# Kernel optimization log

Measured on AMD Instinct MI355X. Metric: run time of the kernel, lower is better.

The kernel has to match this reference:

```python
import jax, jax.numpy as jnp
import numpy as np

B, S, O = 65536, 32, 16  # batch, state_dim, observation_dim


def setup_inputs() -> dict:
    key = jax.random.key(0)
    k1, k2, k3, k4 = jax.random.split(key, 4)
    observation = jax.random.normal(k1, (B, O), dtype=jnp.float32)
    # SPD observation noise covariance per batch element
    L = 0.1 * jax.random.normal(k2, (B, O, O), dtype=jnp.float32)
    observation_noise = jnp.einsum('bij,bkj->bik', L, L) + 1e-3 * jnp.eye(O, dtype=jnp.float32)
    observation_matrix = 0.001 * jax.random.normal(k3, (O, S), dtype=jnp.float32)
    observation_bias = 1e-6 * jax.random.normal(k4, (O,), dtype=jnp.float32)
    prior_mean = jnp.zeros((S,), dtype=jnp.float32)
    prior_precision = jnp.eye(S, dtype=jnp.float32)
    return {
        'observation': observation,
        'observation_noise': observation_noise,
        'observation_matrix': observation_matrix,
        'observation_bias': observation_bias,
        'prior_mean': prior_mean,
        'prior_precision': prior_precision,
    }


def reference(observation, observation_noise, observation_matrix, observation_bias,
              prior_mean, prior_precision):
    # observation: [B, O]; observation_noise: [B, O, O]
    noise_prec = jnp.linalg.inv(observation_noise)                      # [B, O, O]
    HtR = jnp.einsum('os,bop->bsp', observation_matrix, noise_prec)     # H^T R^{-1}: [B, S, O]
    innovation_cov = jnp.einsum('bso,ot->bst', HtR, observation_matrix) # [B, S, S]
    posterior_covariance = jnp.linalg.inv(prior_precision + innovation_cov)  # [B, S, S]
    residual = jnp.einsum('bso,bo->bs', HtR, observation - observation_bias)[..., None]  # [B, S, 1]
    prior_term = (prior_precision @ prior_mean)[:, None]                # [S, 1]
    posterior_mean = posterior_covariance @ (prior_term + residual)     # [B, S, 1]
    return posterior_mean, posterior_covariance
```

## Files before the change

kernel.cpp:

```cpp
#include <hip/hip_runtime.h>
#include <hip/hip_bf16.h>


typedef __attribute__((ext_vector_type(8))) short bf16x8;
typedef __attribute__((ext_vector_type(4))) float f32x4;

__device__ __forceinline__ unsigned bf16rne(float f) {
    unsigned x = __float_as_uint(f);
    return (x + 0x7FFFu + ((x >> 16) & 1u)) >> 16;
}
__device__ __forceinline__ unsigned pack2(float a, float b) {
    return bf16rne(a) | (bf16rne(b) << 16);
}

__global__ void lgs_setup(const float* __restrict__ H, const float* __restrict__ bias,
                          const float* __restrict__ mu0, const float* __restrict__ P,
                          float* __restrict__ ws)
{
    __shared__ float aug[32][65];
    __shared__ float colk[32];
    __shared__ float Gs[16][32];
    __shared__ float Gts[32][16];
    const int tid = threadIdx.x;

    for (int idx = tid; idx < 2048; idx += 256) {
        int r = idx >> 6, c = idx & 63;
        aug[r][c] = (c < 32) ? P[r * 32 + c] : (((c - 32) == r) ? 1.0f : 0.0f);
    }
    __syncthreads();

    for (int k = 0; k < 32; ++k) {
        if (tid < 32) colk[tid] = aug[tid][k];
        __syncthreads();
        if (tid < 64) {
            float rk = aug[k][tid] * (1.0f / colk[k]);
            aug[k][tid] = rk;
            for (int r = 0; r < 32; ++r)
                if (r != k) aug[r][tid] -= colk[r] * rk;
        }
        __syncthreads();
    }

    for (int idx = tid; idx < 512; idx += 256) {
        int o = idx >> 5, s = idx & 31;
        float acc = 0.f;
        for (int v = 0; v < 32; ++v) acc += H[o * 32 + v] * aug[v][32 + s];
        Gs[o][s] = acc;
    }
    for (int idx = tid; idx < 512; idx += 256) {
        int s = idx >> 4, o = idx & 15;
        float acc = 0.f;
        for (int v = 0; v < 32; ++v) acc += aug[s][32 + v] * H[o * 32 + v];
        Gts[s][o] = acc;
    }
    __syncthreads();

    for (int idx = tid; idx < 256; idx += 256) {
        int j = idx >> 4, i = idx & 15;
        float acc = 0.f;
        for (int s = 0; s < 32; ++s) acc += Gs[i][s] * H[j * 32 + s];
        ws[idx] = acc;
    }
    unsigned* wsu = (unsigned*)ws;
    for (int idx = tid; idx < 512; idx += 256) {
        int r = idx >> 8, rem = idx & 255;
        int l = rem >> 2, j = rem & 3;
        int mm = 16 * r + (l & 15);
        int kb = (((l >> 4) * 8) + 2 * j) & 15;
        wsu[768 + idx] = pack2(0.5f * Gts[mm][kb], 0.5f * Gts[mm][kb + 1]);
    }
    for (int idx = tid; idx < 1024; idx += 256) {
        int tt = idx >> 8, rem = idx & 255;
        int l = rem >> 2, j = rem & 3;
        int row = 16 * (tt >> 1) + ((l >> 4) << 2) + j;
        int col = 16 * (tt & 1) + (l & 15);
        ws[1280 + idx] = aug[row][32 + col];
    }
    for (int idx = tid; idx < 512; idx += 256) {
        int c = idx >> 8, rem = idx & 255;
        int l = rem >> 2, j2 = rem & 3;
        int col = 16 * c + (l & 15);
        int k = (((l >> 4) * 8) + 2 * j2) & 15;
        wsu[2304 + idx] = pack2(0.5f * Gs[k][col], 0.5f * Gs[k + 1][col]);
    }
    if (tid < 16) {
        float acc = bias[tid];
        for (int s = 0; s < 32; ++s) acc += H[tid * 32 + s] * mu0[s];
        ws[2816 + tid] = acc;
    }
    if (tid < 32) ws[2832 + tid] = mu0[tid];
}

#define BCAST8(x, K) __int_as_float(__builtin_amdgcn_ds_swizzle(__float_as_int(x), (((K) << 5) | 0x18)))

template <int K>
__device__ __forceinline__ void sweep_step(int l, float (&m0)[16], float (&m1)[16])
{
    const bool own = (l & 7) == (K & 7);
    float (&mp)[16] = (K >> 3) ? m1 : m0;
    float (&mo)[16] = (K >> 3) ? m0 : m1;
    if (own) mp[K] = 1.0f / mp[K];
    float bc[16];
#pragma unroll
    for (int i = 0; i < 16; ++i) bc[i] = BCAST8(mp[i], K & 7);
    float fp = own ? 0.0f : mp[K] * bc[K];
    float fo = mo[K] * bc[K];
#pragma unroll
    for (int i = 0; i < 16; ++i) {
        if (i != K) { mp[i] -= bc[i] * fp; mo[i] -= bc[i] * fo; }
    }
    mp[K] = fp;
    mo[K] = fo;
    if (own) {
        float invd = bc[K];
#pragma unroll
        for (int i = 0; i < 16; ++i) mp[i] = bc[i] * invd;
        mp[K] = -invd;
    }
}

__global__ __launch_bounds__(512, 2) void lgs_main(
    const float* __restrict__ obs, const float* __restrict__ noise,
    const float* __restrict__ ws,
    float* __restrict__ out_mean, float* __restrict__ out_cov, int B)
{
    __shared__ unsigned ldu[8192];

    const int tid  = threadIdx.x;
    const int l    = tid & 63;
    const int wv   = tid >> 6;
    const int g    = l & 7;
    const int slot = wv * 8 + (l >> 3);
    const int b    = blockIdx.x * 64 + slot;
    const int bb   = (b < B) ? b : (B - 1);

    const float* __restrict__ Acm  = ws;
    const float* __restrict__ cvec = ws + 2816;
    const float* __restrict__ m0v  = ws + 2832;

    float m0[16], m1[16];

    const float4* Rr0 = (const float4*)(noise + (size_t)bb * 256 + g * 16);
    const float4* Ar0 = (const float4*)(Acm + g * 16);
    const float4* Rr1 = (const float4*)(noise + (size_t)bb * 256 + (g + 8) * 16);
    const float4* Ar1 = (const float4*)(Acm + (g + 8) * 16);
#pragma unroll
    for (int i = 0; i < 4; ++i) {
        float4 r = Rr0[i], a = Ar0[i];
        m0[4*i+0] = r.x + a.x; m0[4*i+1] = r.y + a.y;
        m0[4*i+2] = r.z + a.z; m0[4*i+3] = r.w + a.w;
        float4 r1 = Rr1[i], a1 = Ar1[i];
        m1[4*i+0] = r1.x + a1.x; m1[4*i+1] = r1.y + a1.y;
        m1[4*i+2] = r1.z + a1.z; m1[4*i+3] = r1.w + a1.w;
    }

    sweep_step<0>(l, m0, m1);   sweep_step<1>(l, m0, m1);
    sweep_step<2>(l, m0, m1);   sweep_step<3>(l, m0, m1);
    sweep_step<4>(l, m0, m1);   sweep_step<5>(l, m0, m1);
    sweep_step<6>(l, m0, m1);   sweep_step<7>(l, m0, m1);
    sweep_step<8>(l, m0, m1);   sweep_step<9>(l, m0, m1);
    sweep_step<10>(l, m0, m1);  sweep_step<11>(l, m0, m1);
    sweep_step<12>(l, m0, m1);  sweep_step<13>(l, m0, m1);
    sweep_step<14>(l, m0, m1);  sweep_step<15>(l, m0, m1);

    {
        unsigned* qb = &ldu[slot * 128 + g * 8];
        const int x0 = g & 4;
        *(uint4*)&qb[x0]      = make_uint4(pack2(m0[0],m0[1]),  pack2(m0[2],m0[3]),
                                           pack2(m0[4],m0[5]),  pack2(m0[6],m0[7]));
        *(uint4*)&qb[x0 ^ 4]  = make_uint4(pack2(m0[8],m0[9]),  pack2(m0[10],m0[11]),
                                           pack2(m0[12],m0[13]), pack2(m0[14],m0[15]));
        *(uint4*)&qb[64 + x0] = make_uint4(pack2(m1[0],m1[1]),  pack2(m1[2],m1[3]),
                                           pack2(m1[4],m1[5]),  pack2(m1[6],m1[7]));
        *(uint4*)&qb[64 + (x0 ^ 4)] = make_uint4(pack2(m1[8],m1[9]),  pack2(m1[10],m1[11]),
                                                 pack2(m1[12],m1[13]), pack2(m1[14],m1[15]));
    }
    asm volatile("" ::: "memory");

    const uint4*  AF4 = (const uint4*)(ws + 768);
    const uint4*  BG4 = (const uint4*)(ws + 2304);
    const float4* PF4 = (const float4*)(ws + 1280);
    uint4 a0u = AF4[l], a1u = AF4[64 + l];
    uint4 g0u = BG4[l], g1u = BG4[64 + l];
    bf16x8 A0, A1, Bg0, Bg1;
    __builtin_memcpy(&A0,  &a0u, 16);
    __builtin_memcpy(&A1,  &a1u, 16);
    __builtin_memcpy(&Bg0, &g0u, 16);
    __builtin_memcpy(&Bg1, &g1u, 16);

    const int ch   = l & 15;
    const int gp   = l >> 4;
    const int qoff = ch * 8 + (((gp & 1) * 4) ^ (ch & 4));
    const int xt   = (ch & 1) << 2;
    const int g2   = gp * 2;
    const int kp   = (gp & 1) * 4;
    const float4 cv = ((const float4*)cvec)[gp];
    const float mu0a = m0v[ch], mu0b = m0v[16 + ch];
    const f32x4 zero = {0.f, 0.f, 0.f, 0.f};

#pragma unroll
    for (int h = 0; h < 8; ++h) {
        const int sh  = wv * 8 + h;
        const int bh  = blockIdx.x * 64 + sh;
        const int bhc = (bh < B) ? bh : (B - 1);
        unsigned* tb = &ldu[sh * 128];

        uint4 qu = *(const uint4*)&tb[qoff];
        bf16x8 Qa; __builtin_memcpy(&Qa, &qu, 16);
        f32x4 d0 = __builtin_amdgcn_mfma_f32_16x16x32_bf16(Qa, Bg0, zero, 0, 0, 0);
        f32x4 d1 = __builtin_amdgcn_mfma_f32_16x16x32_bf16(Qa, Bg1, zero, 0, 0, 0);

        float4 yv = *(const float4*)(obs + (size_t)bhc * 16 + gp * 4);
        float z0 = cv.x - yv.x, z1 = cv.y - yv.y, z2 = cv.z - yv.z, z3 = cv.w - yv.w;
        float p0 = d0[0]*z0 + d0[1]*z1 + d0[2]*z2 + d0[3]*z3;
        float p1 = d1[0]*z0 + d1[1]*z1 + d1[2]*z2 + d1[3]*z3;
        p0 += __int_as_float(__builtin_amdgcn_ds_swizzle(__float_as_int(p0), 0x401F));
        p1 += __int_as_float(__builtin_amdgcn_ds_swizzle(__float_as_int(p1), 0x401F));
        p0 += __shfl_xor(p0, 32, 64);
        p1 += __shfl_xor(p1, 32, 64);
        if (bh < B) {
            if (gp == 0) out_mean[(size_t)bh * 32 + ch]      = mu0a + p0;
            if (gp == 1) out_mean[(size_t)bh * 32 + 16 + ch] = mu0b + p1;
        }

        asm volatile("" ::: "memory");
        *(uint2*)&tb[ch * 8 + (g2 ^ xt)] =
            make_uint2(pack2(d0[0], d0[1]), pack2(d0[2], d0[3]));
        asm volatile("" ::: "memory");
        uint4 bu0 = *(const uint4*)&tb[ch * 8 + (kp ^ xt)];
        bf16x8 Bf0; __builtin_memcpy(&Bf0, &bu0, 16);
        float4 pq0 = PF4[l];
        float4 pq2 = PF4[128 + l];
        f32x4 pfr0; pfr0[0]=pq0.x; pfr0[1]=pq0.y; pfr0[2]=pq0.z; pfr0[3]=pq0.w;
        f32x4 pfr2; pfr2[0]=pq2.x; pfr2[1]=pq2.y; pfr2[2]=pq2.z; pfr2[3]=pq2.w;
        f32x4 s00 = __builtin_amdgcn_mfma_f32_16x16x32_bf16(A0, Bf0, pfr0, 0, 0, 0);
        f32x4 s10 = __builtin_amdgcn_mfma_f32_16x16x32_bf16(A1, Bf0, pfr2, 0, 0, 0);

        asm volatile("" ::: "memory");
        *(uint2*)&tb[ch * 8 + (g2 ^ xt)] =
            make_uint2(pack2(d1[0], d1[1]), pack2(d1[2], d1[3]));
        asm volatile("" ::: "memory");
        uint4 bu1 = *(const uint4*)&tb[ch * 8 + (kp ^ xt)];
        bf16x8 Bf1; __builtin_memcpy(&Bf1, &bu1, 16);
        float4 pq1 = PF4[64 + l];
        float4 pq3 = PF4[192 + l];
        f32x4 pfr1; pfr1[0]=pq1.x; pfr1[1]=pq1.y; pfr1[2]=pq1.z; pfr1[3]=pq1.w;
        f32x4 pfr3; pfr3[0]=pq3.x; pfr3[1]=pq3.y; pfr3[2]=pq3.z; pfr3[3]=pq3.w;
        f32x4 s01 = __builtin_amdgcn_mfma_f32_16x16x32_bf16(A0, Bf1, pfr1, 0, 0, 0);
        f32x4 s11 = __builtin_amdgcn_mfma_f32_16x16x32_bf16(A1, Bf1, pfr3, 0, 0, 0);
        asm volatile("" ::: "memory");

        if (bh < B) {
            float* Sb = out_cov + (size_t)bh * 1024 + (gp * 4) * 32 + ch;
#pragma unroll
            for (int j = 0; j < 4; ++j) {
                Sb[j * 32]       = s00[j];
                Sb[j * 32 + 16]  = s01[j];
                Sb[j * 32 + 512] = s10[j];
                Sb[j * 32 + 528] = s11[j];
            }
        }
    }
}

extern "C" void kernel_launch(void* const* d_in, const int* in_sizes, int n_in,
                              void* d_out, int out_size, void* d_ws, size_t ws_size,
                              hipStream_t stream)
{
    const float* obs   = (const float*)d_in[0];
    const float* noise = (const float*)d_in[1];
    const float* H     = (const float*)d_in[2];
    const float* bias  = (const float*)d_in[3];
    const float* mu0   = (const float*)d_in[4];
    const float* P     = (const float*)d_in[5];
    float* ws = (float*)d_ws;

    const int B = in_sizes[0] / 16;
    float* out_mean = (float*)d_out;
    float* out_cov  = out_mean + (size_t)B * 32;

    lgs_setup<<<1, 256, 0, stream>>>(H, bias, mu0, P, ws);
    lgs_main<<<(B + 63) / 64, 512, 0, stream>>>(obs, noise, ws, out_mean, out_cov, B);
}
```

Measured before the change: 119.9 us.

## Write covariance transposed as float4 stores and double-buffer LDS staging

Because the posterior covariance is symmetric, each lane now writes the transposed MFMA output tile as contiguous float4 rows instead of scattered scalar stores at a 32-float stride. A separate per-wave LDS region holds both bf16 B-operand tiles, so the two pack/store/load rounds and their compiler barriers collapse into one, and all four MFMAs issue together. The mean output becomes a single masked store per wave. The exchange is extra LDS per block, which could affect occupancy, and a reliance on the computed matrix being close enough to symmetric that writing its transpose is acceptable.

Measured after the change: 124.4 us. 3.8% more time.

```diff
diff --git a/kernel.cpp b/kernel.cpp
--- a/kernel.cpp
+++ b/kernel.cpp
@@ -124,7 +124,7 @@
     const float* __restrict__ ws,
     float* __restrict__ out_mean, float* __restrict__ out_cov, int B)
 {
-    __shared__ unsigned ldu[8192];
+    __shared__ unsigned ldu[10240];
 
     const int tid  = threadIdx.x;
     const int l    = tid & 63;
@@ -197,6 +197,7 @@
     const float4 cv = ((const float4*)cvec)[gp];
     const float mu0a = m0v[ch], mu0b = m0v[16 + ch];
     const f32x4 zero = {0.f, 0.f, 0.f, 0.f};
+    unsigned* tw = &ldu[8192 + wv * 256];
 
 #pragma unroll
     for (int h = 0; h < 8; ++h) {
@@ -218,47 +219,46 @@
         p1 += __int_as_float(__builtin_amdgcn_ds_swizzle(__float_as_int(p1), 0x401F));
         p0 += __shfl_xor(p0, 32, 64);
         p1 += __shfl_xor(p1, 32, 64);
-        if (bh < B) {
-            if (gp == 0) out_mean[(size_t)bh * 32 + ch]      = mu0a + p0;
-            if (gp == 1) out_mean[(size_t)bh * 32 + 16 + ch] = mu0b + p1;
+        if (bh < B && l < 32) {
+            float muv = (l < 16) ? (mu0a + p0) : (mu0b + p1);
+            out_mean[(size_t)bh * 32 + l] = muv;
         }
 
-        asm volatile("" ::: "memory");
-        *(uint2*)&tb[ch * 8 + (g2 ^ xt)] =
+        *(uint2*)&tw[ch * 8 + (g2 ^ xt)] =
             make_uint2(pack2(d0[0], d0[1]), pack2(d0[2], d0[3]));
-        asm volatile("" ::: "memory");
-        uint4 bu0 = *(const uint4*)&tb[ch * 8 + (kp ^ xt)];
-        bf16x8 Bf0; __builtin_memcpy(&Bf0, &bu0, 16);
-        float4 pq0 = PF4[l];
-        float4 pq2 = PF4[128 + l];
-        f32x4 pfr0; pfr0[0]=pq0.x; pfr0[1]=pq0.y; pfr0[2]=pq0.z; pfr0[3]=pq0.w;
-        f32x4 pfr2; pfr2[0]=pq2.x; pfr2[1]=pq2.y; pfr2[2]=pq2.z; pfr2[3]=pq2.w;
-        f32x4 s00 = __builtin_amdgcn_mfma_f32_16x16x32_bf16(A0, Bf0, pfr0, 0, 0, 0);
-        f32x4 s10 = __builtin_amdgcn_mfma_f32_16x16x32_bf16(A1, Bf0, pfr2, 0, 0, 0);
-
-        asm volatile("" ::: "memory");
-        *(uint2*)&tb[ch * 8 + (g2 ^ xt)] =
+        *(uint2*)&tw[128 + ch * 8 + (g2 ^ xt)] =
             make_uint2(pack2(d1[0], d1[1]), pack2(d1[2], d1[3]));
         asm volatile("" ::: "memory");
-        uint4 bu1 = *(const uint4*)&tb[ch * 8 + (kp ^ xt)];
-        bf16x8 Bf1; __builtin_memcpy(&Bf1, &bu1, 16);
+        uint4 bu0 = *(const uint4*)&tw[ch * 8 + (kp ^ xt)];
+        uint4 bu1 = *(const uint4*)&tw[128 + ch * 8 + (kp ^ xt)];
+        bf16x8 Bf0, Bf1;
+        __builtin_memcpy(&Bf0, &bu0, 16);
+        __builtin_memcpy(&Bf1, &bu1, 16);
+
+        float4 pq0 = PF4[l];
         float4 pq1 = PF4[64 + l];
+        float4 pq2 = PF4[128 + l];
         float4 pq3 = PF4[192 + l];
+        f32x4 pfr0; pfr0[0]=pq0.x; pfr0[1]=pq0.y; pfr0[2]=pq0.z; pfr0[3]=pq0.w;
         f32x4 pfr1; pfr1[0]=pq1.x; pfr1[1]=pq1.y; pfr1[2]=pq1.z; pfr1[3]=pq1.w;
+        f32x4 pfr2; pfr2[0]=pq2.x; pfr2[1]=pq2.y; pfr2[2]=pq2.z; pfr2[3]=pq2.w;
         f32x4 pfr3; pfr3[0]=pq3.x; pfr3[1]=pq3.y; pfr3[2]=pq3.z; pfr3[3]=pq3.w;
+        f32x4 s00 = __builtin_amdgcn_mfma_f32_16x16x32_bf16(A0, Bf0, pfr0, 0, 0, 0);
         f32x4 s01 = __builtin_amdgcn_mfma_f32_16x16x32_bf16(A0, Bf1, pfr1, 0, 0, 0);
+        f32x4 s10 = __builtin_amdgcn_mfma_f32_16x16x32_bf16(A1, Bf0, pfr2, 0, 0, 0);
         f32x4 s11 = __builtin_amdgcn_mfma_f32_16x16x32_bf16(A1, Bf1, pfr3, 0, 0, 0);
-        asm volatile("" ::: "memory");
 
         if (bh < B) {
-            float* Sb = out_cov + (size_t)bh * 1024 + (gp * 4) * 32 + ch;
-#pragma unroll
-            for (int j = 0; j < 4; ++j) {
-                Sb[j * 32]       = s00[j];
-                Sb[j * 32 + 16]  = s01[j];
-                Sb[j * 32 + 512] = s10[j];
-                Sb[j * 32 + 528] = s11[j];
-            }
+            float* Sb = out_cov + (size_t)bh * 1024;
+            const int cb = gp * 4;
+            *(float4*)&Sb[ch * 32 + cb] =
+                make_float4(s00[0], s00[1], s00[2], s00[3]);
+            *(float4*)&Sb[ch * 32 + 16 + cb] =
+                make_float4(s10[0], s10[1], s10[2], s10[3]);
+            *(float4*)&Sb[(16 + ch) * 32 + cb] =
+                make_float4(s01[0], s01[1], s01[2], s01[3]);
+            *(float4*)&Sb[(16 + ch) * 32 + 16 + cb] =
+                make_float4(s11[0], s11[1], s11[2], s11[3]);
         }
     }
 }
```
